# Kernel optimization log

Hardware: AMD Instinct MI355X
Metric: run time of the kernel (lower is better)

Reference implementation:

```python
import jax, jax.numpy as jnp
import numpy as np

N, E, G, D, L = 20000, 320000, 256, 256, 5
EPS = 1e-5


def _bn(h, g, b):
    # BatchNorm1d in training mode: biased batch statistics over the row dim
    m = h.mean(axis=0)
    v = jnp.mean((h - m) ** 2, axis=0)
    return g * (h - m) / jnp.sqrt(v + EPS) + b


def setup_inputs() -> dict:
    key = jax.random.key(0)
    ks = iter(jax.random.split(key, 40))

    def rn(shape, s=0.1):
        return jax.random.normal(next(ks), shape, dtype=jnp.float32) * s

    inp = {}
    inp['x_feats'] = jax.random.randint(next(ks), (N, 6), 0, 4)
    inp['edge_index'] = jax.random.randint(next(ks), (2, E), 0, N)
    inp['edge_attr'] = jax.random.randint(next(ks), (E, 5), 0, 2)
    inp['batch'] = jnp.sort(jax.random.randint(next(ks), (N,), 0, G))
    inp['nt1'] = rn((119, D)); inp['nt2'] = rn((4, D)); inp['nt3'] = rn((7, D))
    inp['nt4'] = rn((8, D)); inp['nt5'] = rn((5, D)); inp['nt6'] = rn((7, D))
    inp['et1'] = rn((L, 5, D)); inp['et2'] = rn((L, 4, D)); inp['et3'] = rn((L, 2, D))
    inp['et4'] = rn((L, 2, D)); inp['et5'] = rn((L, 2, D))
    inp['w1'] = rn((L, 2 * D, D)); inp['b1'] = rn((L, 2 * D))
    inp['w2'] = rn((L, D, 2 * D)); inp['b2'] = rn((L, D))
    inp['bng'] = 1.0 + rn((L, D)); inp['bnb'] = rn((L, D))
    inp['pw'] = rn((3, D, D)); inp['pg'] = 1.0 + rn((3, D)); inp['pb'] = rn((3, D))
    inp['ow1'] = rn((D // 2, D)); inp['ob1'] = rn((D // 2,))
    inp['ow2'] = rn((2, D // 2)); inp['ob2'] = rn((2,))
    return inp


def reference(x_feats, edge_index, edge_attr, batch,
              nt1, nt2, nt3, nt4, nt5, nt6,
              et1, et2, et3, et4, et5,
              w1, b1, w2, b2, bng, bnb,
              pw, pg, pb, ow1, ob1, ow2, ob2):
    n = x_feats.shape[0]
    # atom embedding: sum of 6 feature embeddings -> [N, D]
    h = (nt1[x_feats[:, 0]] + nt2[x_feats[:, 1]] + nt3[x_feats[:, 2]]
         + nt4[x_feats[:, 3]] + nt5[x_feats[:, 4]] + nt6[x_feats[:, 5]])
    src, dst = edge_index[0], edge_index[1]
    for l in range(L):
        # edge embedding for real edges: [E, D]
        e = (et1[l][edge_attr[:, 0]] + et2[l][edge_attr[:, 1]] + et3[l][edge_attr[:, 2]]
             + et4[l][edge_attr[:, 3]] + et5[l][edge_attr[:, 4]])
        # self-loop edges carry attr [4,0,0,0,0]
        self_e = et1[l][4] + et2[l][0] + et3[l][0] + et4[l][0] + et5[l][0]
        # message = x_j + e, scatter-add into destinations; self loops add h + self_e
        aggr = jax.ops.segment_sum(h[src] + e, dst, num_segments=n) + h + self_e
        # GIN MLP update: D -> 2D -> D
        hh = jax.nn.relu(aggr @ w1[l].T + b1[l]) @ w2[l].T + b2[l]
        # batchnorm then relu (dropout=0; the layer==num_layer branch is unreachable)
        h = jax.nn.relu(_bn(hh, bng[l], bnb[l]))
    # global mean pool over graphs
    counts = jax.ops.segment_sum(jnp.ones((n, 1), h.dtype), batch, num_segments=G)
    hg = jax.ops.segment_sum(h, batch, num_segments=G) / jnp.maximum(counts, 1.0)
    # proj head: (Linear no-bias, BN, ReLU) x2, then Linear no-bias + BN
    for i in range(3):
        hg = _bn(hg @ pw[i].T, pg[i], pb[i])
        if i < 2:
            hg = jax.nn.relu(hg)
    # output MLP: Linear -> Softplus -> Linear
    return jax.nn.softplus(hg @ ow1.T + ob1) @ ow2.T + ob2
```

## Files before the change

kernel.cpp:

```cpp
#include <hip/hip_runtime.h>

#define DD 256
#define TWO_D 512
#define NLAYER 5
#define NGRAPH 256
#define BNEPS 1e-5f

typedef __attribute__((ext_vector_type(8))) _Float16 half8;
typedef __attribute__((ext_vector_type(4))) _Float16 half4;
typedef __attribute__((ext_vector_type(4))) float f32x4;
typedef __attribute__((address_space(1))) void gvoid_t;
typedef __attribute__((address_space(3))) void svoid_t;

__global__ __launch_bounds__(256) void prep_kernel(
    const int* __restrict__ xf,
    const float* __restrict__ nt1, const float* __restrict__ nt2,
    const float* __restrict__ nt3, const float* __restrict__ nt4,
    const float* __restrict__ nt5, const float* __restrict__ nt6,
    _Float16* __restrict__ h16,
    const float* __restrict__ w1, const float* __restrict__ w2,
    _Float16* __restrict__ w1h, _Float16* __restrict__ w2h,
    const float* __restrict__ et1, const float* __restrict__ et2,
    const float* __restrict__ et3, const float* __restrict__ et4,
    const float* __restrict__ et5, _Float16* __restrict__ etab,
    int* __restrict__ deg, int* __restrict__ zr, int zr_words,
    const int* __restrict__ ei, const int* __restrict__ ea,
    int* __restrict__ packed,
    int N, int E)
{
  const int t = threadIdx.x;
  const int b = blockIdx.x;
  const int B_EMB = N;
  const int B_WC  = 128;
  const int B_ET  = NLAYER * 33;
  const int B_ZR  = 96;

  if (b < B_EMB) {
    int i = b, j = t;
    int x0 = xf[i*6+0], x1 = xf[i*6+1], x2 = xf[i*6+2];
    int x3 = xf[i*6+3], x4 = xf[i*6+4], x5 = xf[i*6+5];
    float v = nt1[x0*DD+j] + nt2[x1*DD+j] + nt3[x2*DD+j]
            + nt4[x3*DD+j] + nt5[x4*DD+j] + nt6[x5*DD+j];
    h16[(size_t)i*DD + j] = (_Float16)v;
  } else if (b < B_EMB + B_WC) {
    int bid = b - B_EMB;
    int n = NLAYER * TWO_D * DD;
    for (int i = bid*256 + t; i < n; i += B_WC*256) {
      w1h[i] = (_Float16)w1[i];
      w2h[i] = (_Float16)w2[i];
    }
  } else if (b < B_EMB + B_WC + B_ET) {
    int bid = b - B_EMB - B_WC;
    int l = bid / 33, c = bid % 33;
    int j = t;
    int a0 = (c==32)?4:(c&1);
    int a1 = (c==32)?0:((c>>1)&1);
    int a2 = (c==32)?0:((c>>2)&1);
    int a3 = (c==32)?0:((c>>3)&1);
    int a4 = (c==32)?0:((c>>4)&1);
    etab[((size_t)l*33 + c)*DD + j] = (_Float16)(
        et1[(l*5+a0)*DD+j] + et2[(l*4+a1)*DD+j] + et3[(l*2+a2)*DD+j]
      + et4[(l*2+a3)*DD+j] + et5[(l*2+a4)*DD+j]);
  } else if (b < B_EMB + B_WC + B_ET + B_ZR) {
    int bid = b - B_EMB - B_WC - B_ET;
    int tw = N + zr_words;
    for (int i = bid*256 + t; i < tw; i += B_ZR*256) {
      if (i < N) deg[i] = 0;
      else zr[i - N] = 0;
    }
  } else {
    int bid = b - B_EMB - B_WC - B_ET - B_ZR;
    int e = bid*256 + t;
    if (e < E) {
      int src = ei[e];
      int code = (ea[e*5+0]&1) | ((ea[e*5+1]&1)<<1) | ((ea[e*5+2]&1)<<2)
               | ((ea[e*5+3]&1)<<3) | ((ea[e*5+4]&1)<<4);
      packed[e] = src | (code << 16);
    }
  }
}

__global__ __launch_bounds__(256) void hist_kernel(
    const int* __restrict__ ei, int* __restrict__ deg, int E)
{
  int e = blockIdx.x*256 + threadIdx.x;
  if (e < E) atomicAdd(&deg[ei[E + e]], 1);
}

__global__ __launch_bounds__(1024) void scan_kernel(
    const int* __restrict__ deg, int* __restrict__ row_start,
    int* __restrict__ cursor, int N)
{
  __shared__ int sh[1024];
  int t = threadIdx.x;
  const int CH = (N + 1023) >> 10;
  int base = t * CH;
  int lim = N - base; if (lim < 0) lim = 0; if (lim > CH) lim = CH;
  int s = 0;
  for (int i = 0; i < lim; ++i) s += deg[base + i];
  sh[t] = s;
  __syncthreads();
  for (int off = 1; off < 1024; off <<= 1) {
    int x = (t >= off) ? sh[t - off] : 0;
    __syncthreads();
    sh[t] += x;
    __syncthreads();
  }
  int run = t ? sh[t-1] : 0;
  for (int i = 0; i < lim; ++i) {
    row_start[base+i] = run; cursor[base+i] = run;
    run += deg[base+i];
  }
  if (t == 1023) row_start[N] = sh[1023];
}

__global__ __launch_bounds__(256) void scatter_kernel(
    const int* __restrict__ ei, const int* __restrict__ packed,
    int* __restrict__ cursor, int* __restrict__ esort, int E)
{
  int e = blockIdx.x*256 + threadIdx.x;
  if (e >= E) return;
  int dst = ei[E + e];
  int pos = atomicAdd(&cursor[dst], 1);
  esort[pos] = packed[e];
}

template<int APPLY_BN>
__global__ __launch_bounds__(256) void aggr_kernel(
    const _Float16* __restrict__ hsrc, const _Float16* __restrict__ etab_l,
    const int* __restrict__ row_start, const int* __restrict__ esort,
    const float* __restrict__ stats_prev, const float* __restrict__ g,
    const float* __restrict__ bb, float inv_n,
    _Float16* __restrict__ aggrh, int N)
{
  __shared__ __attribute__((aligned(16))) _Float16 se[33*DD];
  for (int i = threadIdx.x; i < 33*DD/8; i += 256)
    ((int4*)se)[i] = ((const int4*)etab_l)[i];
  __syncthreads();
  const int wave = threadIdx.x >> 6, lane = threadIdx.x & 63;
  const int c4 = lane << 2;
  float sc0=1.f, sc1=1.f, sc2=1.f, sc3=1.f, sh0=0.f, sh1=0.f, sh2=0.f, sh3=0.f;
  if (APPLY_BN) {
#define MKSC(k, SC, SH) { float m_ = stats_prev[c4+k]*inv_n;                      \
    float v_ = fmaxf(stats_prev[DD+c4+k]*inv_n - m_*m_, 0.f);                     \
    SC = g[c4+k]*rsqrtf(v_+BNEPS); SH = bb[c4+k] - m_*SC; }
    MKSC(0, sc0, sh0) MKSC(1, sc1, sh1) MKSC(2, sc2, sh2) MKSC(3, sc3, sh3)
#undef MKSC
  }
  const int W0 = blockIdx.x*4 + wave, NW = gridDim.x*4;

#define BNX(h4, o0, o1, o2, o3)                                           \
  { float t0_ = (float)(h4).x, t1_ = (float)(h4).y,                       \
          t2_ = (float)(h4).z, t3_ = (float)(h4).w;                       \
    if (APPLY_BN) {                                                       \
      t0_ = fmaxf(t0_*sc0 + sh0, 0.f); t1_ = fmaxf(t1_*sc1 + sh1, 0.f);  \
      t2_ = fmaxf(t2_*sc2 + sh2, 0.f); t3_ = fmaxf(t3_*sc3 + sh3, 0.f);  \
    }                                                                     \
    o0 = t0_; o1 = t1_; o2 = t2_; o3 = t3_; }

  for (int node = W0; node < N; node += NW) {
    int p  = row_start[node];
    int pe = row_start[node+1];
    const half4 hv = *(const half4*)(hsrc + (size_t)node*DD + c4);
    const half4 sv = *(const half4*)(se + 32*DD + c4);
    float ax, ay, az, aw;
    BNX(hv, ax, ay, az, aw);
    ax += (float)sv.x; ay += (float)sv.y; az += (float)sv.z; aw += (float)sv.w;
    for (; p + 4 <= pe; p += 4) {
      int pk0 = esort[p], pk1 = esort[p+1], pk2 = esort[p+2], pk3 = esort[p+3];
      const half4 h0 = *(const half4*)(hsrc + (size_t)(pk0 & 0xffff)*DD + c4);
      const half4 h1 = *(const half4*)(hsrc + (size_t)(pk1 & 0xffff)*DD + c4);
      const half4 h2 = *(const half4*)(hsrc + (size_t)(pk2 & 0xffff)*DD + c4);
      const half4 h3 = *(const half4*)(hsrc + (size_t)(pk3 & 0xffff)*DD + c4);
      const half4 e0 = *(const half4*)(se + (pk0 >> 16)*DD + c4);
      const half4 e1 = *(const half4*)(se + (pk1 >> 16)*DD + c4);
      const half4 e2 = *(const half4*)(se + (pk2 >> 16)*DD + c4);
      const half4 e3 = *(const half4*)(se + (pk3 >> 16)*DD + c4);
      float b0x,b0y,b0z,b0w, b1x,b1y,b1z,b1w, b2x,b2y,b2z,b2w, b3x,b3y,b3z,b3w;
      BNX(h0, b0x,b0y,b0z,b0w); BNX(h1, b1x,b1y,b1z,b1w);
      BNX(h2, b2x,b2y,b2z,b2w); BNX(h3, b3x,b3y,b3z,b3w);
      ax += (b0x+(float)e0.x) + (b1x+(float)e1.x) + (b2x+(float)e2.x) + (b3x+(float)e3.x);
      ay += (b0y+(float)e0.y) + (b1y+(float)e1.y) + (b2y+(float)e2.y) + (b3y+(float)e3.y);
      az += (b0z+(float)e0.z) + (b1z+(float)e1.z) + (b2z+(float)e2.z) + (b3z+(float)e3.z);
      aw += (b0w+(float)e0.w) + (b1w+(float)e1.w) + (b2w+(float)e2.w) + (b3w+(float)e3.w);
    }
    for (; p < pe; ++p) {
      int pk = esort[p];
      const half4 hx = *(const half4*)(hsrc + (size_t)(pk & 0xffff)*DD + c4);
      const half4 ex = *(const half4*)(se + (pk >> 16)*DD + c4);
      float bx, by, bz, bw;
      BNX(hx, bx, by, bz, bw);
      ax += bx + (float)ex.x; ay += by + (float)ex.y;
      az += bz + (float)ex.z; aw += bw + (float)ex.w;
    }
    half4 o;
    o.x = (_Float16)ax; o.y = (_Float16)ay; o.z = (_Float16)az; o.w = (_Float16)aw;
    *(half4*)(aggrh + (size_t)node*DD + c4) = o;
  }
#undef BNX
}

template<int RELU, int STATS>
__global__ __launch_bounds__(256) void gemm_bt(
    const _Float16* __restrict__ A,
    const _Float16* __restrict__ B,
    const float* __restrict__ bias,
    _Float16* __restrict__ O,
    float* __restrict__ stats,
    int K, int Nw, int Nreal)
{
  __shared__ __attribute__((aligned(16))) _Float16 smem[8192];
  _Float16* lA = smem;
  _Float16* lB = smem + 4096;
  const int NT = Nw >> 7;
  const int bm = blockIdx.x / NT, bn = blockIdx.x % NT;
  const int m0 = bm << 7, n0 = bn << 7;
  const int t = threadIdx.x;
  const int wave = t >> 6, lane = t & 63;
  const int wm = wave & 1, wn = wave >> 1;
  const int r15 = lane & 15, quad = lane >> 4;
  const int srow = lane >> 2, sq = (lane & 3) << 3;
  f32x4 acc[4][4] = {};
  for (int k0 = 0; k0 < K; k0 += 32) {
    __syncthreads();
#pragma unroll
    for (int i = 0; i < 2; ++i) {
      const int seg = wave*2 + i;
      const int row = seg*16 + srow;
      __builtin_amdgcn_global_load_lds((gvoid_t*)(A + (size_t)(m0+row)*K + k0 + sq),
                                       (svoid_t*)(lA + seg*512), 16, 0, 0);
      __builtin_amdgcn_global_load_lds((gvoid_t*)(B + (size_t)(n0+row)*K + k0 + sq),
                                       (svoid_t*)(lB + seg*512), 16, 0, 0);
    }
    __syncthreads();
    half8 af[4], bfr[4];
#pragma unroll
    for (int f = 0; f < 4; ++f) {
      af[f]  = *(const half8*)(lA + (((wm<<6) + (f<<4) + r15) << 5) + (quad<<3));
      bfr[f] = *(const half8*)(lB + (((wn<<6) + (f<<4) + r15) << 5) + (quad<<3));
    }
#pragma unroll
    for (int fm = 0; fm < 4; ++fm)
#pragma unroll
      for (int fn = 0; fn < 4; ++fn)
        acc[fm][fn] = __builtin_amdgcn_mfma_f32_16x16x32_f16(af[fm], bfr[fn], acc[fm][fn], 0, 0, 0);
  }
  float bv[4];
#pragma unroll
  for (int fn = 0; fn < 4; ++fn) bv[fn] = bias[n0 + (wn<<6) + (fn<<4) + r15];
  __syncthreads();
  _Float16* tb = smem;
#pragma unroll
  for (int fn = 0; fn < 4; ++fn) {
    float s1 = 0.f, s2 = 0.f;
#pragma unroll
    for (int fm = 0; fm < 4; ++fm) {
      const int lr = (wm<<6) + (fm<<4) + (quad<<2);
#pragma unroll
      for (int r = 0; r < 4; ++r) {
        float v = acc[fm][fn][r] + bv[fn];
        if (RELU) v = fmaxf(v, 0.f);
        tb[(lr + r)*40 + (wn<<4) + r15] = (_Float16)v;
        if (STATS && (m0 + lr + r < Nreal)) { s1 += v; s2 += v*v; }
      }
    }
    if (STATS) {
      s1 += __shfl_xor(s1, 16); s1 += __shfl_xor(s1, 32);
      s2 += __shfl_xor(s2, 16); s2 += __shfl_xor(s2, 32);
      if (lane < 16) {
        const int col = n0 + (wn<<6) + (fn<<4) + r15;
        atomicAdd(&stats[col], s1); atomicAdd(&stats[DD + col], s2);
      }
    }
    __syncthreads();
#pragma unroll
    for (int it = 0; it < 2; ++it) {
      int p = t + (it << 8);
      int row = p & 127, strip = (p >> 7) & 1, hsel = p >> 8;
      half8 vv = *(const half8*)(tb + row*40 + (strip<<4) + (hsel<<3));
      *(half8*)(O + (size_t)(m0+row)*Nw + n0 + (strip<<6) + (fn<<4) + (hsel<<3)) = vv;
    }
    __syncthreads();
  }
}

__global__ __launch_bounds__(256) void pool_kernel(
    const _Float16* __restrict__ hh16, const float* __restrict__ stats_prev,
    const float* __restrict__ g, const float* __restrict__ bb, float inv_n,
    const int* __restrict__ batch,
    float* __restrict__ hgsum, int* __restrict__ hgcnt, int N)
{
  int j = threadIdx.x;
  float m = stats_prev[j]*inv_n;
  float var = fmaxf(stats_prev[DD+j]*inv_n - m*m, 0.f);
  float sc = g[j]*rsqrtf(var + BNEPS);
  float sh = bb[j] - m*sc;
  int r0 = blockIdx.x * 64;
  int cur = -1; float acc = 0.f; int run = 0;
  for (int r = 0; r < 64; ++r) {
    int row = r0 + r;
    if (row >= N) break;
    int gg = batch[row];
    if (gg != cur) {
      if (cur >= 0) {
        atomicAdd(&hgsum[(size_t)cur*DD + j], acc);
        if (j == 0) atomicAdd(&hgcnt[cur], run);
      }
      cur = gg; acc = 0.f; run = 0;
    }
    float v = (float)hh16[(size_t)row*DD + j];
    acc += fmaxf(v*sc + sh, 0.f);
    run++;
  }
  if (cur >= 0) {
    atomicAdd(&hgsum[(size_t)cur*DD + j], acc);
    if (j == 0) atomicAdd(&hgcnt[cur], run);
  }
}

template<int MODE>
__global__ __launch_bounds__(256) void proj_gemm_kernel(
    const float* __restrict__ in, const int* __restrict__ cnt,
    const float* __restrict__ pstat_prev,
    const float* __restrict__ gprev, const float* __restrict__ bprev,
    const float* __restrict__ W,
    float* __restrict__ outb, float* __restrict__ pstat)
{
  __shared__ float sA[16][17];
  __shared__ float sB[16][17];
  int tx = threadIdx.x, ty = threadIdx.y;
  int r = blockIdx.y*16 + ty;
  int c = blockIdx.x*16 + tx;
  float acc = 0.f;
  for (int k0 = 0; k0 < DD; k0 += 16) {
    int k = k0 + tx;
    float a = in[(size_t)r*DD + k];
    if (MODE == 0) {
      a /= (float)max(cnt[r], 1);
    } else {
      float m = pstat_prev[k] * (1.0f/NGRAPH);
      float var = fmaxf(pstat_prev[DD + k] * (1.0f/NGRAPH) - m*m, 0.f);
      float sc = gprev[k] * rsqrtf(var + BNEPS);
      a = fmaxf((a - m)*sc + bprev[k], 0.f);
    }
    sA[ty][tx] = a;
    sB[ty][tx] = W[(size_t)(blockIdx.x*16 + ty)*DD + k0 + tx];
    __syncthreads();
#pragma unroll
    for (int kk = 0; kk < 16; ++kk) acc += sA[ty][kk] * sB[tx][kk];
    __syncthreads();
  }
  outb[(size_t)r*DD + c] = acc;
  sA[ty][tx] = acc; sB[ty][tx] = acc*acc;
  __syncthreads();
  for (int o = 8; o > 0; o >>= 1) {
    if (ty < o) { sA[ty][tx] += sA[ty+o][tx]; sB[ty][tx] += sB[ty+o][tx]; }
    __syncthreads();
  }
  if (ty == 0) { atomicAdd(&pstat[c], sA[0][tx]); atomicAdd(&pstat[DD + c], sB[0][tx]); }
}

__global__ __launch_bounds__(128) void out_kernel(
    const float* __restrict__ t2, const float* __restrict__ pstat2,
    const float* __restrict__ g2, const float* __restrict__ b2p,
    const float* __restrict__ ow1, const float* __restrict__ ob1,
    const float* __restrict__ ow2, const float* __restrict__ ob2,
    float* __restrict__ outp)
{
  __shared__ float rowv[DD];
  __shared__ float z[128];
  int r = blockIdx.x, t = threadIdx.x;
#pragma unroll
  for (int half = 0; half < 2; ++half) {
    int j = t + half*128;
    float m = pstat2[j] * (1.0f/NGRAPH);
    float var = fmaxf(pstat2[DD + j] * (1.0f/NGRAPH) - m*m, 0.f);
    float sc = g2[j] * rsqrtf(var + BNEPS);
    rowv[j] = (t2[(size_t)r*DD + j] - m)*sc + b2p[j];
  }
  __syncthreads();
  float a = ob1[t];
  for (int k = 0; k < DD; ++k) a += rowv[k] * ow1[(size_t)t*DD + k];
  z[t] = fmaxf(a, 0.f) + log1pf(expf(-fabsf(a)));
  __syncthreads();
  if (t < 2) {
    float o = ob2[t];
    for (int k = 0; k < 128; ++k) o += z[k] * ow2[t*128 + k];
    outp[r*2 + t] = o;
  }
}

extern "C" void kernel_launch(void* const* d_in, const int* in_sizes, int n_in,
                              void* d_out, int out_size, void* d_ws, size_t ws_size,
                              hipStream_t stream)
{
  const int* x_feats = (const int*)d_in[0];
  const int* ei      = (const int*)d_in[1];
  const int* ea      = (const int*)d_in[2];
  const int* batch   = (const int*)d_in[3];
  const float* nt1 = (const float*)d_in[4];
  const float* nt2 = (const float*)d_in[5];
  const float* nt3 = (const float*)d_in[6];
  const float* nt4 = (const float*)d_in[7];
  const float* nt5 = (const float*)d_in[8];
  const float* nt6 = (const float*)d_in[9];
  const float* et1 = (const float*)d_in[10];
  const float* et2 = (const float*)d_in[11];
  const float* et3 = (const float*)d_in[12];
  const float* et4 = (const float*)d_in[13];
  const float* et5 = (const float*)d_in[14];
  const float* w1  = (const float*)d_in[15];
  const float* b1  = (const float*)d_in[16];
  const float* w2  = (const float*)d_in[17];
  const float* b2  = (const float*)d_in[18];
  const float* bng = (const float*)d_in[19];
  const float* bnb = (const float*)d_in[20];
  const float* pw  = (const float*)d_in[21];
  const float* pg  = (const float*)d_in[22];
  const float* pb  = (const float*)d_in[23];
  const float* ow1 = (const float*)d_in[24];
  const float* ob1 = (const float*)d_in[25];
  const float* ow2 = (const float*)d_in[26];
  const float* ob2 = (const float*)d_in[27];

  const int N = in_sizes[0] / 6;
  const int E = in_sizes[1] / 2;
  const int Mp = ((N + 127) >> 7) << 7;

  unsigned char* wp = (unsigned char*)d_ws;
  size_t off = 0;
  auto carve = [&](size_t bytes) -> void* {
    void* p = wp + off;
    off += (bytes + 255) & ~(size_t)255;
    return p;
  };

  _Float16* h16      = (_Float16*)carve((size_t)N * DD * 2);
  _Float16* aggrh    = (_Float16*)carve((size_t)Mp * DD * 2);
  _Float16* hh16     = (_Float16*)carve((size_t)Mp * DD * 2);
  _Float16* hidh     = (_Float16*)carve((size_t)Mp * TWO_D * 2);
  _Float16* w1h      = (_Float16*)carve((size_t)NLAYER * TWO_D * DD * 2);
  _Float16* w2h      = (_Float16*)carve((size_t)NLAYER * TWO_D * DD * 2);
  _Float16* etabg    = (_Float16*)carve((size_t)NLAYER * 33 * DD * 2);
  int* deg           = (int*)carve((size_t)N * 4);
  int* row_start     = (int*)carve((size_t)(N + 1) * 4);
  int* cursor        = (int*)carve((size_t)N * 4);
  int* packed        = (int*)carve((size_t)E * 4);
  int* esort         = (int*)carve((size_t)E * 4);
  float* stats       = (float*)carve((size_t)NLAYER * 2 * DD * 4);
  float* hgsum       = (float*)carve((size_t)NGRAPH * DD * 4);
  int* hgcnt         = (int*)carve((size_t)NGRAPH * 4);
  float* pstats      = (float*)carve(3 * 2 * DD * 4);
  const int ZR_WORDS = NLAYER*2*DD + NGRAPH*DD + NGRAPH + 3*2*DD;
  float* hgA         = (float*)carve((size_t)NGRAPH * DD * 4);
  float* hgB         = (float*)carve((size_t)NGRAPH * DD * 4);
  float* t0c         = (float*)carve((size_t)NGRAPH * DD * 4);
  (void)ws_size; (void)n_in; (void)out_size;

  const int EB = (E + 255) / 256;
  const float inv_n = 1.0f / (float)N;

  const int PREP_BLOCKS = N + 128 + NLAYER*33 + 96 + EB;
  prep_kernel<<<PREP_BLOCKS, 256, 0, stream>>>(
      x_feats, nt1, nt2, nt3, nt4, nt5, nt6, h16,
      w1, w2, w1h, w2h,
      et1, et2, et3, et4, et5, etabg,
      deg, (int*)stats, ZR_WORDS,
      ei, ea, packed, N, E);
  hist_kernel<<<EB, 256, 0, stream>>>(ei, deg, E);
  scan_kernel<<<1, 1024, 0, stream>>>(deg, row_start, cursor, N);
  scatter_kernel<<<EB, 256, 0, stream>>>(ei, packed, cursor, esort, E);

  const int gm = Mp >> 7;
  for (int l = 0; l < NLAYER; ++l) {
    float* st_prev = stats + (size_t)(l-1)*2*DD;
    float* st_cur  = stats + (size_t)l*2*DD;
    if (l == 0) {
      aggr_kernel<0><<<2048, 256, 0, stream>>>(h16, etabg, row_start, esort,
                                               nullptr, nullptr, nullptr, inv_n,
                                               aggrh, N);
    } else {
      aggr_kernel<1><<<2048, 256, 0, stream>>>(hh16, etabg + (size_t)l*33*DD,
                                               row_start, esort,
                                               st_prev, bng + (l-1)*DD, bnb + (l-1)*DD,
                                               inv_n, aggrh, N);
    }
    gemm_bt<1,0><<<gm * (TWO_D >> 7), 256, 0, stream>>>(
        aggrh, w1h + (size_t)l*TWO_D*DD, b1 + l*TWO_D, hidh, nullptr,
        DD, TWO_D, N);
    gemm_bt<0,1><<<gm * (DD >> 7), 256, 0, stream>>>(
        hidh, w2h + (size_t)l*DD*TWO_D, b2 + l*DD, hh16, st_cur,
        TWO_D, DD, N);
  }

  pool_kernel<<<(N + 63) / 64, 256, 0, stream>>>(
      hh16, stats + (size_t)(NLAYER-1)*2*DD, bng + (NLAYER-1)*DD, bnb + (NLAYER-1)*DD,
      inv_n, batch, hgsum, hgcnt, N);

  dim3 pgrid(16, 16), pblk(16, 16);
  proj_gemm_kernel<0><<<pgrid, pblk, 0, stream>>>(
      hgsum, hgcnt, nullptr, nullptr, nullptr,
      pw + 0*DD*DD, hgA, pstats + 0*2*DD);
  proj_gemm_kernel<1><<<pgrid, pblk, 0, stream>>>(
      hgA, nullptr, pstats + 0*2*DD, pg + 0*DD, pb + 0*DD,
      pw + 1*DD*DD, hgB, pstats + 1*2*DD);
  proj_gemm_kernel<1><<<pgrid, pblk, 0, stream>>>(
      hgB, nullptr, pstats + 1*2*DD, pg + 1*DD, pb + 1*DD,
      pw + 2*DD*DD, t0c, pstats + 2*2*DD);
  out_kernel<<<NGRAPH, 128, 0, stream>>>(
      t0c, pstats + 2*2*DD, pg + 2*DD, pb + 2*DD,
      ow1, ob1, ow2, ob2, (float*)d_out);
}
```

Before: 586.2 us.

## Load GEMM fragments directly from global memory and stage the full output tile in LDS

```diff
diff --git a/kernel.cpp b/kernel.cpp
--- a/kernel.cpp
+++ b/kernel.cpp
@@ -9,8 +9,6 @@
 typedef __attribute__((ext_vector_type(8))) _Float16 half8;
 typedef __attribute__((ext_vector_type(4))) _Float16 half4;
 typedef __attribute__((ext_vector_type(4))) float f32x4;
-typedef __attribute__((address_space(1))) void gvoid_t;
-typedef __attribute__((address_space(3))) void svoid_t;
 
 __global__ __launch_bounds__(256) void prep_kernel(
     const int* __restrict__ xf,
@@ -200,18 +198,16 @@
 #undef BNX
 }
 
-template<int RELU, int STATS>
+template<int RELU, int STATS, int K>
 __global__ __launch_bounds__(256) void gemm_bt(
     const _Float16* __restrict__ A,
     const _Float16* __restrict__ B,
     const float* __restrict__ bias,
     _Float16* __restrict__ O,
     float* __restrict__ stats,
-    int K, int Nw, int Nreal)
-{
-  __shared__ __attribute__((aligned(16))) _Float16 smem[8192];
-  _Float16* lA = smem;
-  _Float16* lB = smem + 4096;
+    int Nw, int Nreal)
+{
+  __shared__ __attribute__((aligned(16))) _Float16 tb[128*132];
   const int NT = Nw >> 7;
   const int bm = blockIdx.x / NT, bn = blockIdx.x % NT;
   const int m0 = bm << 7, n0 = bn << 7;
@@ -219,48 +215,39 @@
   const int wave = t >> 6, lane = t & 63;
   const int wm = wave & 1, wn = wave >> 1;
   const int r15 = lane & 15, quad = lane >> 4;
-  const int srow = lane >> 2, sq = (lane & 3) << 3;
+
+  const _Float16* Ab = A + (size_t)(m0 + (wm<<6) + r15)*K + (quad<<3);
+  const _Float16* Bb = B + (size_t)(n0 + (wn<<6) + r15)*K + (quad<<3);
+
   f32x4 acc[4][4] = {};
+#pragma unroll 2
   for (int k0 = 0; k0 < K; k0 += 32) {
-    __syncthreads();
-#pragma unroll
-    for (int i = 0; i < 2; ++i) {
-      const int seg = wave*2 + i;
-      const int row = seg*16 + srow;
-      __builtin_amdgcn_global_load_lds((gvoid_t*)(A + (size_t)(m0+row)*K + k0 + sq),
-                                       (svoid_t*)(lA + seg*512), 16, 0, 0);
-      __builtin_amdgcn_global_load_lds((gvoid_t*)(B + (size_t)(n0+row)*K + k0 + sq),
-                                       (svoid_t*)(lB + seg*512), 16, 0, 0);
-    }
-    __syncthreads();
-    half8 af[4], bfr[4];
+    half8 af[4], bf[4];
 #pragma unroll
     for (int f = 0; f < 4; ++f) {
-      af[f]  = *(const half8*)(lA + (((wm<<6) + (f<<4) + r15) << 5) + (quad<<3));
-      bfr[f] = *(const half8*)(lB + (((wn<<6) + (f<<4) + r15) << 5) + (quad<<3));
+      af[f] = *(const half8*)(Ab + (size_t)(f<<4)*K + k0);
+      bf[f] = *(const half8*)(Bb + (size_t)(f<<4)*K + k0);
     }
 #pragma unroll
     for (int fm = 0; fm < 4; ++fm)
 #pragma unroll
       for (int fn = 0; fn < 4; ++fn)
-        acc[fm][fn] = __builtin_amdgcn_mfma_f32_16x16x32_f16(af[fm], bfr[fn], acc[fm][fn], 0, 0, 0);
-  }
-  float bv[4];
-#pragma unroll
-  for (int fn = 0; fn < 4; ++fn) bv[fn] = bias[n0 + (wn<<6) + (fn<<4) + r15];
-  __syncthreads();
-  _Float16* tb = smem;
+        acc[fm][fn] = __builtin_amdgcn_mfma_f32_16x16x32_f16(af[fm], bf[fn], acc[fm][fn], 0, 0, 0);
+  }
+
 #pragma unroll
   for (int fn = 0; fn < 4; ++fn) {
+    const int col = (wn<<6) + (fn<<4) + r15;
+    const float bv = bias[n0 + col];
     float s1 = 0.f, s2 = 0.f;
 #pragma unroll
     for (int fm = 0; fm < 4; ++fm) {
       const int lr = (wm<<6) + (fm<<4) + (quad<<2);
 #pragma unroll
       for (int r = 0; r < 4; ++r) {
-        float v = acc[fm][fn][r] + bv[fn];
+        float v = acc[fm][fn][r] + bv;
         if (RELU) v = fmaxf(v, 0.f);
-        tb[(lr + r)*40 + (wn<<4) + r15] = (_Float16)v;
+        tb[(lr + r)*132 + col] = (_Float16)v;
         if (STATS && (m0 + lr + r < Nreal)) { s1 += v; s2 += v*v; }
       }
     }
@@ -268,19 +255,17 @@
       s1 += __shfl_xor(s1, 16); s1 += __shfl_xor(s1, 32);
       s2 += __shfl_xor(s2, 16); s2 += __shfl_xor(s2, 32);
       if (lane < 16) {
-        const int col = n0 + (wn<<6) + (fn<<4) + r15;
-        atomicAdd(&stats[col], s1); atomicAdd(&stats[DD + col], s2);
+        atomicAdd(&stats[n0 + col], s1); atomicAdd(&stats[DD + n0 + col], s2);
       }
     }
-    __syncthreads();
-#pragma unroll
-    for (int it = 0; it < 2; ++it) {
-      int p = t + (it << 8);
-      int row = p & 127, strip = (p >> 7) & 1, hsel = p >> 8;
-      half8 vv = *(const half8*)(tb + row*40 + (strip<<4) + (hsel<<3));
-      *(half8*)(O + (size_t)(m0+row)*Nw + n0 + (strip<<6) + (fn<<4) + (hsel<<3)) = vv;
-    }
-    __syncthreads();
+  }
+  __syncthreads();
+#pragma unroll
+  for (int it = 0; it < 8; ++it) {
+    int idx = (it << 8) + t;
+    int row = idx >> 4, c8 = idx & 15;
+    half8 vv = *(const half8*)(tb + row*132 + (c8<<3));
+    *(half8*)(O + (size_t)(m0+row)*Nw + n0 + (c8<<3)) = vv;
   }
 }
 
@@ -485,12 +470,12 @@
                                                st_prev, bng + (l-1)*DD, bnb + (l-1)*DD,
                                                inv_n, aggrh, N);
     }
-    gemm_bt<1,0><<<gm * (TWO_D >> 7), 256, 0, stream>>>(
+    gemm_bt<1,0,DD><<<gm * (TWO_D >> 7), 256, 0, stream>>>(
         aggrh, w1h + (size_t)l*TWO_D*DD, b1 + l*TWO_D, hidh, nullptr,
-        DD, TWO_D, N);
-    gemm_bt<0,1><<<gm * (DD >> 7), 256, 0, stream>>>(
+        TWO_D, N);
+    gemm_bt<0,1,TWO_D><<<gm * (DD >> 7), 256, 0, stream>>>(
         hidh, w2h + (size_t)l*DD*TWO_D, b2 + l*DD, hh16, st_cur,
-        TWO_D, DD, N);
+        DD, N);
   }
 
   pool_kernel<<<(N + 63) / 64, 256, 0, stream>>>(
```

Result: slower. 682.9 us (+16.5%).
